# Optimization experiments

Measured on AMD Instinct MI355X. Metric: run time of the kernel, lower is better.

The kernel has to match this reference:

```python
import jax, jax.numpy as jnp
import numpy as np

BETA_MIN = 0.1
BETA_MAX = 20.0

def _marginals(t):
    # VP-SDE closed forms: mean(t) = exp(-0.25 t^2 (bmax-bmin) - 0.5 t bmin), std = sqrt(1 - mean^2)
    log_mean = -0.25 * t ** 2 * (BETA_MAX - BETA_MIN) - 0.5 * t * BETA_MIN
    mean = jnp.exp(log_mean)
    std = jnp.sqrt(jnp.maximum(1.0 - jnp.exp(2.0 * log_mean), 1e-12))
    return mean, std

def setup_inputs() -> dict:
    key = jax.random.key(0)
    k1, k2, k3 = jax.random.split(key, 3)
    N, M, D = 4096, 16384, 128
    x = jax.random.normal(k1, (N, D), dtype=jnp.float32)
    t = jax.random.uniform(k2, (N,), dtype=jnp.float32, minval=0.05, maxval=1.0)
    train_data = jax.random.normal(k3, (M, D), dtype=jnp.float32)
    return {"x": x, "t": t, "train_data": train_data}

def reference(x, t, train_data):
    # x: (N, D), t: (N,), train_data: (M, D)
    mean, sigma = _marginals(t)                       # (N,), (N,)
    inv_var = 1.0 / (sigma ** 2)                      # (N,)
    # logpdf[n, i] = -0.5 * ||x_n - mean_n * y_i||^2 / sigma_n^2
    # expanded: ||x_n||^2 - 2 mean_n <x_n, y_i> + mean_n^2 ||y_i||^2
    xy = jnp.einsum('nd,md->nm', x, train_data)       # (N, M) GEMM
    x2 = jnp.sum(x ** 2, axis=1)                      # (N,)
    y2 = jnp.sum(train_data ** 2, axis=1)             # (M,)
    sq = x2[:, None] - 2.0 * mean[:, None] * xy + (mean ** 2)[:, None] * y2[None, :]
    logpdf = -0.5 * sq * inv_var[:, None]             # (N, M)
    weights = jax.nn.softmax(logpdf, axis=1)          # (N, M)
    evals = weights @ train_data                      # (N, D)
    evals = jnp.where(jnp.isnan(evals), 0.0, evals)
    return (evals - x) * inv_var[:, None]
```

## Files before the change

kernel.cpp:

```cpp
#include <hip/hip_runtime.h>

typedef unsigned int u32;
typedef unsigned short u16;
typedef short s16x8 __attribute__((ext_vector_type(8)));
typedef float f32x4 __attribute__((ext_vector_type(4)));

#define BETA_MIN 0.1f
#define BETA_MAX 20.0f

#define MFMA16(a, b, c) __builtin_amdgcn_mfma_f32_16x16x32_bf16(a, b, c, 0, 0, 0)

__device__ __forceinline__ u16 f2bf(float f) {
    u32 u = __float_as_uint(f);
    u32 r = u + 0x7FFFu + ((u >> 16) & 1u);
    return (u16)(r >> 16);
}
__device__ __forceinline__ float bf2f(u16 h) {
    return __uint_as_float(((u32)h) << 16);
}
__device__ __forceinline__ f32x4 zero4() {
    f32x4 z = {0.f, 0.f, 0.f, 0.f};
    return z;
}

template <int CTRL>
__device__ __forceinline__ float dppf(float x) {
    return __int_as_float(__builtin_amdgcn_update_dpp(
        0, __float_as_int(x), CTRL, 0xF, 0xF, false));
}
__device__ __forceinline__ float rowmax16(float x) {
    x = fmaxf(x, dppf<0xB1>(x));
    x = fmaxf(x, dppf<0x4E>(x));
    x = fmaxf(x, dppf<0x124>(x));
    x = fmaxf(x, dppf<0x128>(x));
    return x;
}
__device__ __forceinline__ float rowsum16(float x) {
    x += dppf<0xB1>(x);
    x += dppf<0x4E>(x);
    x += dppf<0x124>(x);
    x += dppf<0x128>(x);
    return x;
}


__global__ void rows_kernel(const float* __restrict__ t, float* __restrict__ rowc, int N) {
    int n = blockIdx.x * blockDim.x + threadIdx.x;
    if (n >= N) return;
    float tv   = t[n];
    float lm   = -0.25f * tv * tv * (BETA_MAX - BETA_MIN) - 0.5f * tv * BETA_MIN;
    float mean = __expf(lm);
    float e2   = __expf(2.0f * lm);
    float s2   = fmaxf(1.0f - e2, 1e-12f);
    float iv   = 1.0f / s2;
    rowc[n * 4 + 0] = mean * iv;
    rowc[n * 4 + 1] = -0.5f * mean * mean * iv;
    rowc[n * 4 + 2] = iv;
    rowc[n * 4 + 3] = 0.f;
}

__global__ void conv_hilo(const float* __restrict__ src, u16* __restrict__ hi,
                          u16* __restrict__ lo, int total4) {
    int idx = blockIdx.x * blockDim.x + threadIdx.x;
    if (idx >= total4) return;
    float4 v = ((const float4*)src)[idx];
    float f[4] = {v.x, v.y, v.z, v.w};
    u32 hp[2], lp[2];
    u16 h[4], l[4];
#pragma unroll
    for (int j = 0; j < 4; ++j) {
        h[j] = f2bf(f[j]);
        l[j] = f2bf(f[j] - bf2f(h[j]));
    }
    hp[0] = (u32)h[0] | ((u32)h[1] << 16);
    hp[1] = (u32)h[2] | ((u32)h[3] << 16);
    lp[0] = (u32)l[0] | ((u32)l[1] << 16);
    lp[1] = (u32)l[2] | ((u32)l[3] << 16);
    ((uint2*)hi)[idx] = make_uint2(hp[0], hp[1]);
    ((uint2*)lo)[idx] = make_uint2(lp[0], lp[1]);
}

__global__ __launch_bounds__(256)
void vt_y2_kernel(const float* __restrict__ train, u16* __restrict__ Vt,
                  float* __restrict__ y2, int M) {
    __shared__ u16 T[128][66];
    const int t = threadIdx.x;
    const int m0 = blockIdx.x * 64;
    const int g = t >> 5, ln = t & 31;
#pragma unroll
    for (int i = 0; i < 8; ++i) {
        int lr = i * 8 + g;
        const float* row = train + (size_t)(m0 + lr) * 128;
        float acc = 0.f;
#pragma unroll
        for (int j = 0; j < 4; ++j) {
            float v = row[ln + 32 * j];
            T[ln + 32 * j][lr] = f2bf(v);
            acc += v * v;
        }
#pragma unroll
        for (int d = 16; d >= 1; d >>= 1) acc += __shfl_xor(acc, d, 32);
        if (ln == 0) y2[m0 + lr] = acc;
    }
    __syncthreads();
#pragma unroll
    for (int i = 0; i < 4; ++i) {
        int c = i * 256 + t;
        int d = c >> 3, mo = (c & 7) * 8;
        u32 w0 = *(const u32*)&T[d][mo + 0];
        u32 w1 = *(const u32*)&T[d][mo + 2];
        u32 w2 = *(const u32*)&T[d][mo + 4];
        u32 w3 = *(const u32*)&T[d][mo + 6];
        *(uint4*)(Vt + (size_t)d * M + m0 + mo) = make_uint4(w0, w1, w2, w3);
    }
}

__global__ __launch_bounds__(256, 4)
void flash_kernel(const u16* __restrict__ Khi, const u16* __restrict__ Klo,
                  const u16* __restrict__ Vt,  const u16* __restrict__ Qhi,
                  const u16* __restrict__ Qlo, const float* __restrict__ rowc,
                  const float* __restrict__ y2, float* __restrict__ partO,
                  float* __restrict__ partML, int N, int M, int mchunk) {
    __shared__ u16 sKhi[32][136];
    __shared__ u16 sKlo[32][136];
    __shared__ u16 sVt[128][40];
    __shared__ u16 sP[4][16][40];

    const int tid  = threadIdx.x;
    const int wave = tid >> 6, lane = tid & 63;
    const int l15  = lane & 15, quad = lane >> 4;
    const int qb = blockIdx.x, chunk = blockIdx.y;
    const int q0 = qb * 64 + wave * 16;
    const int m_begin = chunk * mchunk;

    s16x8 qh[4], ql[4];
    {
        int row = q0 + l15;
        const u16* ph = Qhi + (size_t)row * 128;
        const u16* pl = Qlo + (size_t)row * 128;
#pragma unroll
        for (int kb = 0; kb < 4; ++kb) {
            qh[kb] = *(const s16x8*)(ph + kb * 32 + quad * 8);
            ql[kb] = *(const s16x8*)(pl + kb * 32 + quad * 8);
        }
    }
    float av[4], bv[4];
#pragma unroll
    for (int k = 0; k < 4; ++k) {
        int r = q0 + quad * 4 + k;
        av[k] = rowc[r * 4 + 0];
        bv[k] = rowc[r * 4 + 1];
    }

    f32x4 O[8];
#pragma unroll
    for (int db = 0; db < 8; ++db) O[db] = zero4();
    float m_run[4], l_run[4];
#pragma unroll
    for (int k = 0; k < 4; ++k) { m_run[k] = -INFINITY; l_run[k] = 0.f; }

    for (int mt = 0; mt < mchunk; mt += 32) {
        const int m0 = m_begin + mt;
        __syncthreads();
#pragma unroll
        for (int r = 0; r < 2; ++r) {
            int c = tid + r * 256;
            int row = c >> 4, col = (c & 15) * 8;
            *(uint4*)&sKhi[row][col] = *(const uint4*)(Khi + (size_t)(m0 + row) * 128 + col);
            *(uint4*)&sKlo[row][col] = *(const uint4*)(Klo + (size_t)(m0 + row) * 128 + col);
            int dd = c >> 2, mc = (c & 3) * 8;
            *(uint4*)&sVt[dd][mc] = *(const uint4*)(Vt + (size_t)dd * M + m0 + mc);
        }
        __syncthreads();

        float y2v0 = y2[m0 + l15];
        float y2v1 = y2[m0 + 16 + l15];

        f32x4 S[2];
        S[0] = zero4(); S[1] = zero4();
#pragma unroll
        for (int kb = 0; kb < 4; ++kb) {
            s16x8 bh0 = *(const s16x8*)&sKhi[l15][kb * 32 + quad * 8];
            s16x8 bh1 = *(const s16x8*)&sKhi[16 + l15][kb * 32 + quad * 8];
            s16x8 bl0 = *(const s16x8*)&sKlo[l15][kb * 32 + quad * 8];
            s16x8 bl1 = *(const s16x8*)&sKlo[16 + l15][kb * 32 + quad * 8];
            S[0] = MFMA16(qh[kb], bh0, S[0]);
            S[0] = MFMA16(ql[kb], bh0, S[0]);
            S[0] = MFMA16(qh[kb], bl0, S[0]);
            S[1] = MFMA16(qh[kb], bh1, S[1]);
            S[1] = MFMA16(ql[kb], bh1, S[1]);
            S[1] = MFMA16(qh[kb], bl1, S[1]);
        }

#pragma unroll
        for (int k = 0; k < 4; ++k) {
            float s0 = av[k] * S[0][k] + bv[k] * y2v0;
            float s1 = av[k] * S[1][k] + bv[k] * y2v1;
            float rm    = rowmax16(fmaxf(s0, s1));
            float mnew  = fmaxf(m_run[k], rm);
            float alpha = __expf(m_run[k] - mnew);
            float p0 = __expf(s0 - mnew);
            float p1 = __expf(s1 - mnew);
            m_run[k] = mnew;
            l_run[k] = l_run[k] * alpha + (p0 + p1);
            sP[wave][quad * 4 + k][l15]      = f2bf(p0);
            sP[wave][quad * 4 + k][16 + l15] = f2bf(p1);
#pragma unroll
            for (int db = 0; db < 8; ++db) O[db][k] *= alpha;
        }
        asm volatile("s_waitcnt lgkmcnt(0)" ::: "memory");

        s16x8 pa = *(const s16x8*)&sP[wave][l15][quad * 8];
#pragma unroll
        for (int db = 0; db < 8; ++db) {
            s16x8 vb = *(const s16x8*)&sVt[db * 16 + l15][quad * 8];
            O[db] = MFMA16(pa, vb, O[db]);
        }
    }

#pragma unroll
    for (int db = 0; db < 8; ++db) {
#pragma unroll
        for (int k = 0; k < 4; ++k) {
            int row = q0 + quad * 4 + k;
            partO[((size_t)chunk * N + row) * 128 + db * 16 + l15] = O[db][k];
        }
    }
#pragma unroll
    for (int k = 0; k < 4; ++k) {
        float lsum = rowsum16(l_run[k]);
        if (l15 == 0) {
            int row = q0 + quad * 4 + k;
            partML[((size_t)chunk * N + row) * 2 + 0] = m_run[k];
            partML[((size_t)chunk * N + row) * 2 + 1] = lsum;
        }
    }
}

__global__ void combine_kernel(const float* __restrict__ partO, const float* __restrict__ partML,
                               const float* __restrict__ x, const float* __restrict__ rowc,
                               float* __restrict__ out, int N, int split) {
    int n = blockIdx.x, d = threadIdx.x;
    float Mx = -INFINITY;
    for (int c = 0; c < split; ++c)
        Mx = fmaxf(Mx, partML[((size_t)c * N + n) * 2]);
    float L = 0.f, acc = 0.f;
    for (int c = 0; c < split; ++c) {
        float w = __expf(partML[((size_t)c * N + n) * 2] - Mx);
        L   += w * partML[((size_t)c * N + n) * 2 + 1];
        acc += w * partO[((size_t)c * N + n) * 128 + d];
    }
    float evals = acc / L;
    if (evals != evals) evals = 0.f;
    float iv = rowc[n * 4 + 2];
    out[(size_t)n * 128 + d] = (evals - x[(size_t)n * 128 + d]) * iv;
}

extern "C" void kernel_launch(void* const* d_in, const int* in_sizes, int n_in,
                              void* d_out, int out_size, void* d_ws, size_t ws_size,
                              hipStream_t stream) {
    const float* x     = (const float*)d_in[0];
    const float* t     = (const float*)d_in[1];
    const float* train = (const float*)d_in[2];
    float* out = (float*)d_out;

    const int N = in_sizes[1];
    const int D = 128;
    const int M = in_sizes[2] / D;

    char* ws = (char*)d_ws;
    size_t off = 0;
    auto alloc = [&](size_t bytes) -> void* {
        void* p = ws + off;
        off = (off + bytes + 255) & ~(size_t)255;
        return p;
    };
    u16* Khi   = (u16*)alloc((size_t)M * D * 2);
    u16* Klo   = (u16*)alloc((size_t)M * D * 2);
    u16* Vt    = (u16*)alloc((size_t)M * D * 2);
    u16* Qhi   = (u16*)alloc((size_t)N * D * 2);
    u16* Qlo   = (u16*)alloc((size_t)N * D * 2);
    float* rowc = (float*)alloc((size_t)N * 16);
    float* y2   = (float*)alloc((size_t)M * 4);
    size_t base = off;
    size_t per  = (size_t)N * D * 4 + (size_t)N * 8 + 512;
    int split = 16;
    while (split > 1 && base + per * split > ws_size) split >>= 1;
    float* partO  = (float*)alloc((size_t)split * N * D * 4);
    float* partML = (float*)alloc((size_t)split * N * 8);

    rows_kernel<<<(N + 255) / 256, 256, 0, stream>>>(t, rowc, N);
    conv_hilo<<<(N * D / 4 + 255) / 256, 256, 0, stream>>>(x, Qhi, Qlo, N * D / 4);
    conv_hilo<<<(M * D / 4 + 255) / 256, 256, 0, stream>>>(train, Khi, Klo, M * D / 4);
    vt_y2_kernel<<<M / 64, 256, 0, stream>>>(train, Vt, y2, M);

    int mchunk = M / split;
    dim3 grid(N / 64, split);
    flash_kernel<<<grid, 256, 0, stream>>>(Khi, Klo, Vt, Qhi, Qlo, rowc, y2,
                                           partO, partML, N, M, mchunk);
    combine_kernel<<<N, 128, 0, stream>>>(partO, partML, x, rowc, out, N, split);
}
```

Baseline: 202.2 us.

## Fuse prep kernels and double flash block to 128 query rows

Merges the row-constant computation into the x hi/lo conversion kernel, and folds the train hi/lo split into the transpose/y2 kernel so train is read once. The flash kernel now uses 512 threads (8 waves, 128 query rows per block), so each loaded K/V tile is shared by twice as many queries. The grid is reordered so chunks of the same query block are adjacent. This cuts launch count and global K/V traffic, at the cost of larger blocks with possibly lower occupancy and scattered 2-byte stores in the train prep.

After: 179.0 us. 11.5% less time.

```diff
diff --git a/kernel.cpp b/kernel.cpp
--- a/kernel.cpp
+++ b/kernel.cpp
@@ -44,24 +44,22 @@
 }
 
 
-__global__ void rows_kernel(const float* __restrict__ t, float* __restrict__ rowc, int N) {
-    int n = blockIdx.x * blockDim.x + threadIdx.x;
-    if (n >= N) return;
-    float tv   = t[n];
-    float lm   = -0.25f * tv * tv * (BETA_MAX - BETA_MIN) - 0.5f * tv * BETA_MIN;
-    float mean = __expf(lm);
-    float e2   = __expf(2.0f * lm);
-    float s2   = fmaxf(1.0f - e2, 1e-12f);
-    float iv   = 1.0f / s2;
-    rowc[n * 4 + 0] = mean * iv;
-    rowc[n * 4 + 1] = -0.5f * mean * mean * iv;
-    rowc[n * 4 + 2] = iv;
-    rowc[n * 4 + 3] = 0.f;
-}
-
-__global__ void conv_hilo(const float* __restrict__ src, u16* __restrict__ hi,
-                          u16* __restrict__ lo, int total4) {
+__global__ void conv_x_rows(const float* __restrict__ src, const float* __restrict__ t,
+                            u16* __restrict__ hi, u16* __restrict__ lo,
+                            float* __restrict__ rowc, int total4, int N) {
     int idx = blockIdx.x * blockDim.x + threadIdx.x;
+    if (idx < N) {
+        float tv   = t[idx];
+        float lm   = -0.25f * tv * tv * (BETA_MAX - BETA_MIN) - 0.5f * tv * BETA_MIN;
+        float mean = __expf(lm);
+        float e2   = __expf(2.0f * lm);
+        float s2   = fmaxf(1.0f - e2, 1e-12f);
+        float iv   = 1.0f / s2;
+        rowc[idx * 4 + 0] = mean * iv;
+        rowc[idx * 4 + 1] = -0.5f * mean * mean * iv;
+        rowc[idx * 4 + 2] = iv;
+        rowc[idx * 4 + 3] = 0.f;
+    }
     if (idx >= total4) return;
     float4 v = ((const float4*)src)[idx];
     float f[4] = {v.x, v.y, v.z, v.w};
@@ -81,8 +79,9 @@
 }
 
 __global__ __launch_bounds__(256)
-void vt_y2_kernel(const float* __restrict__ train, u16* __restrict__ Vt,
-                  float* __restrict__ y2, int M) {
+void train_prep_kernel(const float* __restrict__ train, u16* __restrict__ Khi,
+                       u16* __restrict__ Klo, u16* __restrict__ Vt,
+                       float* __restrict__ y2, int M) {
     __shared__ u16 T[128][66];
     const int t = threadIdx.x;
     const int m0 = blockIdx.x * 64;
@@ -90,17 +89,25 @@
 #pragma unroll
     for (int i = 0; i < 8; ++i) {
         int lr = i * 8 + g;
-        const float* row = train + (size_t)(m0 + lr) * 128;
+        int m  = m0 + lr;
+        const float* row = train + (size_t)m * 128;
+        u16* kh = Khi + (size_t)m * 128;
+        u16* kl = Klo + (size_t)m * 128;
         float acc = 0.f;
 #pragma unroll
         for (int j = 0; j < 4; ++j) {
-            float v = row[ln + 32 * j];
-            T[ln + 32 * j][lr] = f2bf(v);
+            int d = ln + 32 * j;
+            float v = row[d];
+            u16 h = f2bf(v);
+            u16 l = f2bf(v - bf2f(h));
+            T[d][lr] = h;
+            kh[d] = h;
+            kl[d] = l;
             acc += v * v;
         }
 #pragma unroll
         for (int d = 16; d >= 1; d >>= 1) acc += __shfl_xor(acc, d, 32);
-        if (ln == 0) y2[m0 + lr] = acc;
+        if (ln == 0) y2[m] = acc;
     }
     __syncthreads();
 #pragma unroll
@@ -115,7 +122,7 @@
     }
 }
 
-__global__ __launch_bounds__(256, 4)
+__global__ __launch_bounds__(512, 4)
 void flash_kernel(const u16* __restrict__ Khi, const u16* __restrict__ Klo,
                   const u16* __restrict__ Vt,  const u16* __restrict__ Qhi,
                   const u16* __restrict__ Qlo, const float* __restrict__ rowc,
@@ -124,13 +131,13 @@
     __shared__ u16 sKhi[32][136];
     __shared__ u16 sKlo[32][136];
     __shared__ u16 sVt[128][40];
-    __shared__ u16 sP[4][16][40];
+    __shared__ u16 sP[8][16][40];
 
     const int tid  = threadIdx.x;
     const int wave = tid >> 6, lane = tid & 63;
     const int l15  = lane & 15, quad = lane >> 4;
-    const int qb = blockIdx.x, chunk = blockIdx.y;
-    const int q0 = qb * 64 + wave * 16;
+    const int chunk = blockIdx.x, qb = blockIdx.y;
+    const int q0 = qb * 128 + wave * 16;
     const int m_begin = chunk * mchunk;
 
     s16x8 qh[4], ql[4];
@@ -162,13 +169,11 @@
     for (int mt = 0; mt < mchunk; mt += 32) {
         const int m0 = m_begin + mt;
         __syncthreads();
-#pragma unroll
-        for (int r = 0; r < 2; ++r) {
-            int c = tid + r * 256;
-            int row = c >> 4, col = (c & 15) * 8;
+        {
+            int row = tid >> 4, col = (tid & 15) * 8;
             *(uint4*)&sKhi[row][col] = *(const uint4*)(Khi + (size_t)(m0 + row) * 128 + col);
             *(uint4*)&sKlo[row][col] = *(const uint4*)(Klo + (size_t)(m0 + row) * 128 + col);
-            int dd = c >> 2, mc = (c & 3) * 8;
+            int dd = tid >> 2, mc = (tid & 3) * 8;
             *(uint4*)&sVt[dd][mc] = *(const uint4*)(Vt + (size_t)dd * M + m0 + mc);
         }
         __syncthreads();
@@ -289,14 +294,13 @@
     float* partO  = (float*)alloc((size_t)split * N * D * 4);
     float* partML = (float*)alloc((size_t)split * N * 8);
 
-    rows_kernel<<<(N + 255) / 256, 256, 0, stream>>>(t, rowc, N);
-    conv_hilo<<<(N * D / 4 + 255) / 256, 256, 0, stream>>>(x, Qhi, Qlo, N * D / 4);
-    conv_hilo<<<(M * D / 4 + 255) / 256, 256, 0, stream>>>(train, Khi, Klo, M * D / 4);
-    vt_y2_kernel<<<M / 64, 256, 0, stream>>>(train, Vt, y2, M);
+    conv_x_rows<<<(N * D / 4 + 255) / 256, 256, 0, stream>>>(x, t, Qhi, Qlo, rowc,
+                                                             N * D / 4, N);
+    train_prep_kernel<<<M / 64, 256, 0, stream>>>(train, Khi, Klo, Vt, y2, M);
 
     int mchunk = M / split;
-    dim3 grid(N / 64, split);
-    flash_kernel<<<grid, 256, 0, stream>>>(Khi, Klo, Vt, Qhi, Qlo, rowc, y2,
+    dim3 grid(split, N / 128);
+    flash_kernel<<<grid, 512, 0, stream>>>(Khi, Klo, Vt, Qhi, Qlo, rowc, y2,
                                            partO, partML, N, M, mchunk);
     combine_kernel<<<N, 128, 0, stream>>>(partO, partML, x, rowc, out, N, split);
 }
```
